# Performance work log

Hardware: AMD Instinct MI355X
Metric: run time of the kernel (lower is better)

The kernel has to match this reference:

```python
import jax, jax.numpy as jnp
import numpy as np

NQUBIT = 24
CHI = 512
Q = 2
MID_SCALE = 1.0 / 32.0  # 1/sqrt(Q*CHI): keeps the sequential bond-matrix product O(1)


def _to_c(x):
    # x[..., 0] = real part, x[..., 1] = imag part -> complex64
    return jax.lax.complex(x[..., 0], x[..., 1])


def setup_inputs() -> dict:
    key = jax.random.key(0)
    k1, k2, k3 = jax.random.split(key, 3)
    t_first = jax.random.normal(k1, (1, Q, CHI, 2), dtype=jnp.float32)
    t_mid = jax.random.normal(k2, (NQUBIT - 2, CHI, Q, CHI, 2), dtype=jnp.float32) * MID_SCALE
    t_last = jax.random.normal(k3, (CHI, Q, 1, 2), dtype=jnp.float32)
    return {"t_first": t_first, "t_mid": t_mid, "t_last": t_last}


def _sweep(t_first, t_mid, t_last):
    # Faithful translation of center_orthogonalization(c=-1):
    # left-to-right orthogonalize_left2right over sites 0..nqubit-2, dc=-1 (no
    # truncation), normalize=False. Each step: SVD of (Dl*q, Dr) reshape,
    # keep u as the new site tensor, absorb r = diag(s) @ vh into the next site
    # via einsum 'ab,bcd->acd'. Returns the center (last) tensor.
    tensors = [_to_c(t_first)] + [_to_c(t_mid[i]) for i in range(NQUBIT - 2)] + [_to_c(t_last)]
    for i in range(NQUBIT - 1):  # loop over sites (structural, shapes differ per site)
        t = tensors[i]
        Dl, q, Dr = t.shape
        u, s, vh = jnp.linalg.svd(t.reshape(Dl * q, Dr), full_matrices=False)
        tensors[i] = u.reshape(Dl, q, -1)            # left-orthogonal site tensor
        r = s.astype(vh.dtype)[:, None] * vh          # diag(s) @ vh, shape (k, Dr)
        tensors[i + 1] = jnp.einsum('ab,bcd->acd', r, tensors[i + 1])
    c = tensors[-1]  # center tensor, shape (CHI, Q, 1) complex64
    return jnp.stack([jnp.real(c), jnp.imag(c)], axis=-1)  # (CHI, Q, 1, 2) float32


def reference(t_first, t_mid, t_last):
    return _sweep(t_first, t_mid, t_last)
```

## Files before the change

### kernel.cpp

```cpp
#include <hip/hip_runtime.h>
#include <math.h>


#define LDV 513
typedef float2 cplx;

__device__ __forceinline__ cplx cmul(cplx a, cplx b){ return make_float2(a.x*b.x - a.y*b.y, a.x*b.y + a.y*b.x); }
__device__ __forceinline__ cplx cmulc(cplx a, cplx b){  return make_float2(a.x*b.x + a.y*b.y, a.x*b.y - a.y*b.x); }
__device__ __forceinline__ cplx cadd(cplx a, cplx b){ return make_float2(a.x+b.x, a.y+b.y); }
__device__ __forceinline__ cplx csub(cplx a, cplx b){ return make_float2(a.x-b.x, a.y-b.y); }
__device__ __forceinline__ cplx conjc(cplx a){ return make_float2(a.x, -a.y); }

#define EPS_S 5.9604645e-8f
#define UNFL_S 1.17549435e-38f
#define UW 256

__device__ cplx g_A[1024*512];
__device__ cplx g_B[512*512];
__device__ cplx g_VTc[512*512];
__device__ cplx g_R[512*512];
__device__ cplx g_tauf[520];
__device__ cplx g_taup[520];
__device__ float g_d[520], g_e[520];
__device__ float g_VTr[LDV*LDV];
__device__ float g_VT2[LDV*LDV];
__device__ float g_W[LDV*LDV];
__device__ float g_z[520], g_zz[520], g_zorig[520], g_dtmp[520], g_ztmp[520], g_dsig[520];
__device__ double g_root[520];
__device__ int g_idxq[520], g_idx[520], g_idxp[520], g_rowmap[520];
__device__ int g_inode[80], g_ndiml[80], g_ndimr[80];
__device__ float g_sig[520];
__device__ int g_K, g_nlvl_, g_nd_;
__device__ float g_tol_, g_z1_;
__device__ double g_rho_;
__device__ float g_scq[520];
__device__ float g_betaq[520];
__device__ float g_rn[520];
__device__ float g_partC[256];
__device__ float g_partR[256];

__device__ __forceinline__ float wred(float v){
  for (int off=32;off;off>>=1) v+=__shfl_down(v,off);
  return v;
}
__device__ __forceinline__ float reduce256(const float* arr){
  __shared__ float sr[256];
  sr[threadIdx.x]=arr[threadIdx.x];
  __syncthreads();
  for (int s=128;s>0;s>>=1){
    if (threadIdx.x<s) sr[threadIdx.x]+=sr[threadIdx.x+s];
    __syncthreads();
  }
  float v=sr[0];
  __syncthreads();
  return v;
}

struct RfgOut { float beta; cplx tau; cplx scal; int skip; };
__device__ RfgOut clarfg_head(cplx alpha, float xn2){
  RfgOut o;
  if (xn2==0.f && alpha.y==0.f){
    o.beta=alpha.x; o.tau=make_float2(0.f,0.f); o.scal=make_float2(0.f,0.f); o.skip=1;
  } else {
    float anorm=sqrtf(alpha.x*alpha.x+alpha.y*alpha.y+xn2);
    float beta=(alpha.x>=0.f)?-anorm:anorm;
    o.beta=beta;
    o.tau=make_float2((beta-alpha.x)/beta,-alpha.y/beta);
    cplx dd=make_float2(alpha.x-beta,alpha.y);
    float dn=dd.x*dd.x+dd.y*dd.y;
    o.scal=make_float2(dd.x/dn,-dd.y/dn);
    o.skip=0;
  }
  return o;
}

__device__ float slapy2(float x, float y){
  float xa=fabsf(x), ya=fabsf(y);
  float w=fmaxf(xa,ya), z=fminf(xa,ya);
  if (z==0.f) return w;
  float q=z/w; return w*sqrtf(1.f+q*q);
}

__device__ void slartg(float f, float g, float* cs, float* sn, float* r){
  if (g==0.f){ *cs=1.f; *sn=0.f; *r=f; }
  else if (f==0.f){ *cs=0.f; *sn=(g>0.f)?1.f:-1.f; *r=fabsf(g); }
  else {
    float f1=fabsf(f);
    float d=sqrtf(f*f+g*g);
    *cs = f1/d;
    *r = (f>0.f)? d : -d;
    *sn = g / *r;
  }
}

__device__ void slas2(float f, float g, float h, float* ssmin, float* ssmax){
  float fa=fabsf(f), ga=fabsf(g), ha=fabsf(h);
  float fhmn=fminf(fa,ha), fhmx=fmaxf(fa,ha);
  if (fhmn==0.f){
    *ssmin=0.f;
    if (fhmx==0.f) *ssmax=ga;
    else { float mx=fmaxf(fhmx,ga), mn=fminf(fhmx,ga); float q=mn/mx; *ssmax=mx*sqrtf(1.f+q*q); }
  } else {
    if (ga < fhmx){
      float as=1.f+fhmn/fhmx, at=(fhmx-fhmn)/fhmx;
      float au=ga/fhmx; au=au*au;
      float c=2.f/(sqrtf(as*as+au)+sqrtf(at*at+au));
      *ssmin=fhmn*c; *ssmax=fhmx/c;
    } else {
      float au=fhmx/ga;
      if (au==0.f){ *ssmin=(fhmn*fhmx)/ga; *ssmax=ga; }
      else {
        float as=1.f+fhmn/fhmx, at=(fhmx-fhmn)/fhmx;
        float c=1.f/(sqrtf(1.f+(as*au)*(as*au))+sqrtf(1.f+(at*au)*(at*au)));
        *ssmin=(fhmn*c)*au; *ssmin=*ssmin+*ssmin;
        *ssmax=ga/(c+c);
      }
    }
  }
}

__device__ void slasv2(float f, float g, float h, float* ssmin, float* ssmax,
                       float* snr, float* csr, float* snl, float* csl){
  float ft=f, fa=fabsf(f), ht=h, ha=fabsf(h);
  int pmax=1;
  bool swap_=(ha>fa);
  if (swap_){ pmax=3; float t=ft; ft=ht; ht=t; t=fa; fa=ha; ha=t; }
  float gt=g, ga=fabsf(g);
  float clt=0.f, crt=0.f, slt=0.f, srt=0.f;
  if (ga==0.f){ *ssmin=ha; *ssmax=fa; clt=1.f; crt=1.f; slt=0.f; srt=0.f; }
  else {
    bool gasmal=true;
    if (ga>fa){
      pmax=2;
      if ((fa/ga) < EPS_S){
        gasmal=false;
        *ssmax=ga;
        if (ha>1.f) *ssmin=fa/(ga/ha); else *ssmin=(fa/ga)*ha;
        clt=1.f; slt=ht/gt; srt=1.f; crt=ft/gt;
      }
    }
    if (gasmal){
      float d=fa-ha;
      float l=(d==fa)?1.f:(d/fa);
      float mm=gt/ft;
      float t=2.f-l;
      float mm2=mm*mm, tt=t*t;
      float s=sqrtf(tt+mm2);
      float r=(l==0.f)?fabsf(mm):sqrtf(l*l+mm2);
      float a=0.5f*(s+r);
      *ssmin=ha/a; *ssmax=fa*a;
      if (mm2==0.f){
        if (l==0.f) t=copysignf(2.f,ft)*copysignf(1.f,gt);
        else t=gt/copysignf(d,ft)+mm/t;
      } else {
        t=(mm/(s+t)+mm/(r+l))*(1.f+a);
      }
      float l2=sqrtf(t*t+4.f);
      crt=2.f/l2; srt=t/l2;
      clt=(crt+srt*mm)/a;
      slt=(ht/ft)*srt/a;
    }
  }
  if (swap_){ *csl=srt; *snl=crt; *csr=slt; *snr=clt; }
  else      { *csl=clt; *snl=slt; *csr=crt; *snr=srt; }
  float tsign=0.f;
  if (pmax==1) tsign=copysignf(1.f,*csr)*copysignf(1.f,*csl)*copysignf(1.f,f);
  if (pmax==2) tsign=copysignf(1.f,*snr)*copysignf(1.f,*csl)*copysignf(1.f,g);
  if (pmax==3) tsign=copysignf(1.f,*snr)*copysignf(1.f,*snl)*copysignf(1.f,h);
  *ssmax=copysignf(*ssmax,tsign);
  *ssmin=copysignf(*ssmin,tsign*copysignf(1.f,f)*copysignf(1.f,h));
}

__device__ void slasr_f(int mrows, int ncols, const float* c1, const float* s1, float* a, int lda){
  for (int j=1;j<=mrows-1;++j){
    float ct=c1[j], st=s1[j];
    if (ct!=1.f || st!=0.f){
      float* rj=&a[(j-1)*lda]; float* rj1=&a[j*lda];
      for (int i=0;i<ncols;++i){
        float tmp=rj1[i];
        rj1[i]=ct*tmp-st*rj[i];
        rj[i]=st*tmp+ct*rj[i];
      }
    }
  }
}
__device__ void slasr_b(int mrows, int ncols, const float* c1, const float* s1, float* a, int lda){
  for (int j=mrows-1;j>=1;--j){
    float ct=c1[j], st=s1[j];
    if (ct!=1.f || st!=0.f){
      float* rj=&a[(j-1)*lda]; float* rj1=&a[j*lda];
      for (int i=0;i<ncols;++i){
        float tmp=rj1[i];
        rj1[i]=ct*tmp-st*rj[i];
        rj[i]=st*tmp+ct*rj[i];
      }
    }
  }
}

__device__ void sbdsqr_u(int n, int ncvt, float* d, float* e, float* vt, int ldvt){
  const int MAXITR=6;
  if (n==0) return;
  if (n>1){
    int nm1=n-1, nm12=nm1+nm1, nm13=nm12+nm1;
    float wk[112];
    float tolmul=10.f;
    float tol=tolmul*EPS_S;
    float smax=0.f;
    for (int i=1;i<=n;i++) smax=fmaxf(smax,fabsf(d[i]));
    for (int i=1;i<=n-1;i++) smax=fmaxf(smax,fabsf(e[i]));
    float sminl=0.f, thresh;
    {
      float sminoa=fabsf(d[1]);
      if (sminoa!=0.f){
        float mu=sminoa;
        for (int i=2;i<=n;i++){
          mu=fabsf(d[i])*(mu/(mu+fabsf(e[i-1])));
          sminoa=fminf(sminoa,mu);
          if (sminoa==0.f) break;
        }
      }
      sminoa=sminoa/sqrtf((float)n);
      thresh=fmaxf(tol*sminoa,(float)(MAXITR*n*n)*UNFL_S);
    }
    int M=n, iter=0, maxit=MAXITR*n*n;
    int oldll=-1, oldm=-1, idir=0;
    while (1){
      if (M<=1) break;
      if (iter>maxit) break;
      int ll=0; bool split=false;
      smax=fabsf(d[M]);
      for (int lll=1;lll<=M-1;++lll){
        ll=M-lll;
        float abss=fabsf(d[ll]), abse=fabsf(e[ll]);
        if (abse<=thresh){ split=true; break; }
        smax=fmaxf(smax,fmaxf(abss,abse));
      }
      if (!split) ll=0;
      else {
        e[ll]=0.f;
        if (ll==M-1){ M=M-1; continue; }
      }
      ll=ll+1;
      if (ll==M-1){
        float sigmn,sigmx,sinr,cosr,sinl,cosl;
        slasv2(d[M-1],e[M-1],d[M],&sigmn,&sigmx,&sinr,&cosr,&sinl,&cosl);
        d[M-1]=sigmx; e[M-1]=0.f; d[M]=sigmn;
        if (ncvt>0){
          float* x=&vt[(M-2)*ldvt]; float* y=&vt[(M-1)*ldvt];
          for (int c=0;c<ncvt;c++){ float xv=x[c],yv=y[c]; x[c]=cosr*xv+sinr*yv; y[c]=cosr*yv-sinr*xv; }
        }
        M-=2; continue;
      }
      if (ll>oldm || M<oldll) idir=(fabsf(d[ll])>=fabsf(d[M]))?1:2;
      bool conv=false;
      if (idir==1){
        if (fabsf(e[M-1])<=fabsf(tol)*fabsf(d[M])){ e[M-1]=0.f; conv=true; }
        else {
          float mu=fabsf(d[ll]); sminl=mu;
          for (int lll=ll;lll<=M-1;++lll){
            if (fabsf(e[lll])<=tol*mu){ e[lll]=0.f; conv=true; break; }
            mu=fabsf(d[lll+1])*(mu/(mu+fabsf(e[lll])));
            sminl=fminf(sminl,mu);
          }
        }
      } else {
        if (fabsf(e[ll])<=fabsf(tol)*fabsf(d[ll])){ e[ll]=0.f; conv=true; }
        else {
          float mu=fabsf(d[M]); sminl=mu;
          for (int lll=M-1;lll>=ll;--lll){
            if (fabsf(e[lll])<=tol*mu){ e[lll]=0.f; conv=true; break; }
            mu=fabsf(d[lll])*(mu/(mu+fabsf(e[lll])));
            sminl=fminf(sminl,mu);
          }
        }
      }
      if (conv) continue;
      oldll=ll; oldm=M;
      float shift=0.f, rr;
      if ((float)n*tol*(sminl/smax)<=fmaxf(EPS_S,0.01f*tol)) shift=0.f;
      else {
        float sll;
        if (idir==1){ sll=fabsf(d[ll]); slas2(d[M-1],e[M-1],d[M],&shift,&rr); }
        else        { sll=fabsf(d[M]);  slas2(d[ll],e[ll],d[ll+1],&shift,&rr); }
        if (sll>0.f){ float q=shift/sll; if (q*q<EPS_S) shift=0.f; }
      }
      iter += M-ll;
      if (shift==0.f){
        if (idir==1){
          float cs=1.f, oldcs=1.f, sn=0.f, oldsn=0.f;
          for (int i=ll;i<=M-1;++i){
            float c2,r1;
            slartg(d[i]*cs,e[i],&c2,&sn,&r1); cs=c2;
            if (i>ll) e[i-1]=oldsn*r1;
            float oc2;
            slartg(oldcs*r1,d[i+1]*sn,&oc2,&oldsn,&d[i]); oldcs=oc2;
            wk[i-ll+1]=cs; wk[i-ll+1+nm1]=sn;
          }
          float h=d[M]*cs; d[M]=h*oldcs; e[M-1]=h*oldsn;
          if (ncvt>0) slasr_f(M-ll+1,ncvt,wk,wk+nm1,&vt[(ll-1)*ldvt],ldvt);
          if (fabsf(e[M-1])<=thresh) e[M-1]=0.f;
        } else {
          float cs=1.f, oldcs=1.f, sn=0.f, oldsn=0.f;
          for (int i=M;i>=ll+1;--i){
            float c2,r1;
            slartg(d[i]*cs,e[i-1],&c2,&sn,&r1); cs=c2;
            if (i<M) e[i]=oldsn*r1;
            float oc2;
            slartg(oldcs*r1,d[i-1]*sn,&oc2,&oldsn,&d[i]); oldcs=oc2;
            wk[i-ll]=cs; wk[i-ll+nm1]=-sn;
            wk[i-ll+nm12]=oldcs; wk[i-ll+nm13]=-oldsn;
          }
          float h=d[ll]*cs; d[ll]=h*oldcs; e[ll]=h*oldsn;
          if (ncvt>0) slasr_b(M-ll+1,ncvt,wk+nm12,wk+nm13,&vt[(ll-1)*ldvt],ldvt);
          if (fabsf(e[ll])<=thresh) e[ll]=0.f;
        }
      } else {
        if (idir==1){
          float f=(fabsf(d[ll])-shift)*(copysignf(1.f,d[ll])+shift/d[ll]);
          float g=e[ll], cosr,sinr,cosl,sinl,r1;
          for (int i=ll;i<=M-1;++i){
            slartg(f,g,&cosr,&sinr,&r1);
            if (i>ll) e[i-1]=r1;
            f=cosr*d[i]+sinr*e[i];
            e[i]=cosr*e[i]-sinr*d[i];
            g=sinr*d[i+1];
            d[i+1]=cosr*d[i+1];
            slartg(f,g,&cosl,&sinl,&r1);
            d[i]=r1;
            f=cosl*e[i]+sinl*d[i+1];
            d[i+1]=cosl*d[i+1]-sinl*e[i];
            if (i<M-1){ g=sinl*e[i+1]; e[i+1]=cosl*e[i+1]; }
            wk[i-ll+1]=cosr; wk[i-ll+1+nm1]=sinr;
            wk[i-ll+1+nm12]=cosl; wk[i-ll+1+nm13]=sinl;
          }
          e[M-1]=f;
          if (ncvt>0) slasr_f(M-ll+1,ncvt,wk,wk+nm1,&vt[(ll-1)*ldvt],ldvt);
          if (fabsf(e[M-1])<=thresh) e[M-1]=0.f;
        } else {
          float f=(fabsf(d[M])-shift)*(copysignf(1.f,d[M])+shift/d[M]);
          float g=e[M-1], cosr,sinr,cosl,sinl,r1;
          for (int i=M;i>=ll+1;--i){
            slartg(f,g,&cosr,&sinr,&r1);
            if (i<M) e[i]=r1;
            f=cosr*d[i]+sinr*e[i-1];
            e[i-1]=cosr*e[i-1]-sinr*d[i];
            g=sinr*d[i-1];
            d[i-1]=cosr*d[i-1];
            slartg(f,g,&cosl,&sinl,&r1);
            d[i]=r1;
            f=cosl*e[i-1]+sinl*d[i-1];
            d[i-1]=cosl*d[i-1]-sinl*e[i-1];
            if (i>ll+1){ g=sinl*e[i-2]; e[i-2]=cosl*e[i-2]; }
            wk[i-ll]=cosr; wk[i-ll+nm1]=-sinr;
            wk[i-ll+nm12]=cosl; wk[i-ll+nm13]=-sinl;
          }
          e[ll]=f;
          if (fabsf(e[ll])<=thresh) e[ll]=0.f;
          if (ncvt>0) slasr_b(M-ll+1,ncvt,wk+nm12,wk+nm13,&vt[(ll-1)*ldvt],ldvt);
        }
      }
    }
  }
  for (int i=1;i<=n;i++){
    if (d[i]<0.f){
      d[i]=-d[i];
      if (ncvt>0){ float* row=&vt[(i-1)*ldvt]; for (int c=0;c<ncvt;c++) row[c]=-row[c]; }
    }
  }
  for (int i=1;i<=n-1;i++){
    int isub=1; float smin2=d[1];
    for (int j=2;j<=n+1-i;j++){ if (d[j]<=smin2){ isub=j; smin2=d[j]; } }
    if (isub!=n+1-i){
      d[isub]=d[n+1-i]; d[n+1-i]=smin2;
      if (ncvt>0){
        float* a=&vt[(isub-1)*ldvt]; float* b=&vt[(n-i)*ldvt];
        for (int c=0;c<ncvt;c++){ float t=a[c]; a[c]=b[c]; b[c]=t; }
      }
    }
  }
}

__device__ void slasdq_u(int sqre, int n, int ncvt, float* d, float* e, float* vt, int ldvt){
  if (n==0) return;
  float cwk[33], swk[33];
  int np1=n+1;
  if (sqre==1){
    for (int i=1;i<=n-1;i++){
      float cs,sn,r; slartg(d[i],e[i],&cs,&sn,&r);
      d[i]=r; e[i]=sn*d[i+1]; d[i+1]=cs*d[i+1];
      cwk[i]=cs; swk[i]=sn;
    }
    { float cs,sn,r; slartg(d[n],e[n],&cs,&sn,&r);
      d[n]=r; e[n]=0.f; cwk[n]=cs; swk[n]=sn; }
    if (ncvt>0) slasr_f(np1,ncvt,cwk,swk,vt,ldvt);
    for (int i=1;i<=n-1;i++){
      float cs,sn,r; slartg(d[i],e[i],&cs,&sn,&r);
      d[i]=r; e[i]=sn*d[i+1]; d[i+1]=cs*d[i+1];
    }
  }
  sbdsqr_u(n,ncvt,d,e,vt,ldvt);
  for (int i=1;i<=n;i++){
    int isub=i; float smin2=d[i];
    for (int j=i+1;j<=n;j++){ if (d[j]<smin2){ isub=j; smin2=d[j]; } }
    if (isub!=i){
      d[isub]=d[i]; d[i]=smin2;
      if (ncvt>0){
        float* a=&vt[(isub-1)*ldvt]; float* b=&vt[(i-1)*ldvt];
        for (int c=0;c<ncvt;c++){ float t=a[c]; a[c]=b[c]; b[c]=t; }
      }
    }
  }
}

__device__ void slamrg(int n1, int n2, const float* a, int s1, int s2, int* idx){
  int n1sv=n1, n2sv=n2, i=1;
  int ind1=(s1>0)?1:n1;
  int ind2=(s2>0)?(1+n1):(n1+n2);
  while (n1sv>0 && n2sv>0){
    if (a[ind1]<=a[ind2]){ idx[i++]=ind1; ind1+=s1; n1sv--; }
    else { idx[i++]=ind2; ind2+=s2; n2sv--; }
  }
  if (n1sv==0){ for(;n2sv>0;n2sv--){ idx[i++]=ind2; ind2+=s2; } }
  else { for(;n1sv>0;n1sv--){ idx[i++]=ind1; ind1+=s1; } }
}

__device__ void slasdt(int n, int* lvl, int* nd, int* inode, int* ndiml, int* ndimr, int msub){
  int maxn=(n>1)?n:1;
  float temp=logf((float)maxn/(float)(msub+1))/logf(2.f);
  *lvl=(int)temp+1;
  int i=n/2;
  inode[1]=i+1; ndiml[1]=i; ndimr[1]=n-i-1;
  int il=0, ir=1, llst=1;
  for (int nl=1;nl<=*lvl-1;++nl){
    for (int j=0;j<=llst-1;++j){
      il+=2; ir+=2;
      int nc=llst+j;
      ndiml[il]=ndiml[nc]/2;
      ndimr[il]=ndiml[nc]-ndiml[il]-1;
      inode[il]=inode[nc]-ndimr[il]-1;
      ndiml[ir]=ndimr[nc]/2;
      ndimr[ir]=ndimr[nc]-ndiml[ir]-1;
      inode[ir]=inode[nc]+ndiml[ir]+1;
    }
    llst*=2;
  }
  *nd=llst*2-1;
}

__device__ void merge_node(int nl, int nr, int sqre, float* d, int* idxq,
                           float alpha, float beta, float* VT, int ld)
{
  const int tid=threadIdx.x, nth=blockDim.x;
  const int n=nl+nr+1, m=n+sqre, nlp1=nl+1, nlp2=nl+2;
  if (tid==0){
    float* z=g_z;
    float z1=alpha*VT[(nlp1-1)*ld+(nlp1-1)];
    z[1]=z1; g_z1_=z1;
    for (int i=nl;i>=1;--i){
      z[i+1]=alpha*VT[(i-1)*ld+(nlp1-1)];
      d[i+1]=d[i];
      idxq[i+1]=idxq[i]+1;
    }
    for (int i=nlp2;i<=m;++i) z[i]=beta*VT[(i-1)*ld+(nlp2-1)];
    d[1]=0.f;
    for (int i=nlp2;i<=n;++i) idxq[i]+=nlp1;
    for (int i=2;i<=n;++i){ g_dtmp[i]=d[idxq[i]]; g_ztmp[i]=z[idxq[i]]; }
    slamrg(nl,nr,g_dtmp+1,1,1,g_idx+1);
    for (int i=2;i<=n;++i){
      int idxi=1+g_idx[i];
      d[i]=g_dtmp[idxi];
      z[i]=g_ztmp[idxi];
    }
    float tol=fmaxf(fabsf(alpha),fabsf(beta));
    tol=8.f*EPS_S*fmaxf(fabsf(d[n]),tol);
    g_tol_=tol;
    int K=1, K2=n+1, jprev=0, j;
    for (j=2;j<=n;++j){
      if (fabsf(z[j])<=tol){
        K2--; g_idxp[K2]=j;
        if (j==n){ jprev=0; break; }
      } else { jprev=j; break; }
    }
    if (jprev>0){
      j=jprev;
      for (;;){
        j++;
        if (j>n) break;
        if (fabsf(z[j])<=tol){ K2--; g_idxp[K2]=j; }
        else {
          if (fabsf(d[j]-d[jprev])<=tol){
            float s_=z[jprev], c_=z[j];
            float tau_=slapy2(c_,s_);
            c_/=tau_; s_=-s_/tau_;
            z[j]=tau_; z[jprev]=0.f;
            int idxjp=idxq[g_idx[jprev]+1];
            int idxj =idxq[g_idx[j]+1];
            if (idxjp<=nlp1) idxjp--;
            if (idxj <=nlp1) idxj--;
            float* xr=&VT[(idxjp-1)*ld];
            float* yr=&VT[(idxj-1)*ld];
            for (int cc=0;cc<m;++cc){
              float xv=xr[cc], yv=yr[cc];
              xr[cc]=c_*xv+s_*yv;
              yr[cc]=c_*yv-s_*xv;
            }
            K2--; g_idxp[K2]=jprev;
            jprev=j;
          } else {
            K++; g_zz[K]=z[jprev]; g_idxp[K]=jprev;
            jprev=j;
          }
        }
      }
      K++; g_zz[K]=z[jprev]; g_idxp[K]=jprev;
    }
    g_K=K;
    for (int jj=2;jj<=n;++jj){
      g_dsig[jj]=d[g_idxp[jj]];
      int rm=idxq[g_idx[g_idxp[jj]]+1];
      if (rm<=nlp1) rm--;
      g_rowmap[jj]=rm;
    }
  }
  __syncthreads();
  int K=g_K;
  for (int t=tid;t<(n-1)*m;t+=nth){
    int jj=2+t/m, cc=t%m;
    g_VT2[(jj-1)*LDV+cc]=VT[(g_rowmap[jj]-1)*ld+cc];
  }
  __syncthreads();
  if (tid==0){
    float tol=g_tol_;
    g_dsig[1]=0.f;
    float hlftol=tol*0.5f;
    if (fabsf(g_dsig[2])<=hlftol) g_dsig[2]=hlftol;
    float z1=g_z1_;
    float c_=1.f, s_=0.f;
    if (m>n){
      float t1=slapy2(z1,g_z[m]);
      if (t1<=tol){ c_=1.f; s_=0.f; g_z[1]=tol; }
      else { g_z[1]=t1; c_=z1/t1; s_=g_z[m]/t1; }
    } else {
      if (fabsf(z1)<=tol) g_z[1]=tol; else g_z[1]=z1;
    }
    for (int jj=2;jj<=K;++jj) g_z[jj]=g_zz[jj];
    if (m>n){
      for (int i=1;i<=nlp1;++i){
        float v=VT[(nlp1-1)*ld+(i-1)];
        VT[(m-1)*ld+(i-1)]=-s_*v;
        g_VT2[(i-1)]=c_*v;
      }
      for (int i=nlp2;i<=m;++i){
        float v=VT[(m-1)*ld+(i-1)];
        g_VT2[(i-1)]=s_*v;
        VT[(m-1)*ld+(i-1)]=c_*v;
      }
    } else {
      for (int i=1;i<=m;++i) g_VT2[(i-1)]=VT[(nlp1-1)*ld+(i-1)];
    }
    for (int jj=K+1;jj<=n;++jj) d[jj]=g_dsig[jj];
    double rho=0.0;
    for (int jj=1;jj<=K;++jj){ double zz2=(double)g_z[jj]; rho+=zz2*zz2; g_zorig[jj]=g_z[jj]; }
    g_rho_=rho;
  }
  __syncthreads();
  for (int t=tid;t<(n-K)*m;t+=nth){
    int jj=K+1+t/m, cc=t%m;
    VT[(jj-1)*ld+cc]=g_VT2[(jj-1)*LDV+cc];
  }
  __syncthreads();
  if (K==1){
    if (tid==0){
      d[1]=fabsf(g_z[1]);
      for (int cc=0;cc<m;++cc) VT[cc]=g_VT2[cc];
      slamrg(1,n-1,d,1,-1,idxq);
    }
    __syncthreads();
    return;
  }
  {
    double rho=g_rho_;
    for (int i=1+tid;i<=K;i+=nth){
      double di=(double)g_dsig[i];
      double lo=di*di, hi;
      if (i<K){ double dn=(double)g_dsig[i+1]; hi=dn*dn; }
      else { double dn=(double)g_dsig[K]; hi=dn*dn+rho; }
      for (int it=0;it<110;++it){
        double mid=0.5*(lo+hi);
        double f=1.0;
        for (int j=1;j<=K;++j){
          double dj=(double)g_dsig[j];
          double zj=(double)g_z[j];
          f+=zj*zj/(dj*dj-mid);
        }
        if (f>=0.0) hi=mid; else lo=mid;
      }
      g_root[i]=0.5*(lo+hi);
      d[i]=(float)sqrt(g_root[i]);
    }
  }
  __syncthreads();
  for (int i=1+tid;i<=K;i+=nth){
    double di=(double)g_dsig[i], di2=di*di;
    double p=di2-g_root[K];
    for (int j=1;j<=i-1;++j){
      double dj=(double)g_dsig[j];
      p*=(di2-g_root[j])/((di-dj)*(di+dj));
    }
    for (int j=i;j<=K-1;++j){
      double dj1=(double)g_dsig[j+1];
      p*=(di2-g_root[j])/((di-dj1)*(di+dj1));
    }
    g_ztmp[i]=copysignf((float)sqrt(fabs(p)),g_zorig[i]);
  }
  __syncthreads();
  for (int i=1+tid;i<=K;i+=nth) g_z[i]=g_ztmp[i];
  __syncthreads();
  for (int i=1+tid;i<=K;i+=nth){
    double xi=g_root[i];
    double nrm=0.0;
    for (int j=1;j<=K;++j){
      double dj=(double)g_dsig[j];
      double w=(double)g_z[j]/(dj*dj-xi);
      g_W[(i-1)*LDV+(j-1)]=(float)w;
      nrm+=w*w;
    }
    float inv=(float)(1.0/sqrt(nrm));
    for (int j=1;j<=K;++j) g_W[(i-1)*LDV+(j-1)]*=inv;
  }
  __syncthreads();
  for (int t=tid;t<K*m;t+=nth){
    int i=1+t/m, cc=t%m;
    float acc=0.f;
    for (int j=1;j<=K;++j)
      acc=fmaf(g_W[(i-1)*LDV+(j-1)],g_VT2[(j-1)*LDV+cc],acc);
    VT[(i-1)*ld+cc]=acc;
  }
  __syncthreads();
  if (tid==0) slamrg(K,n-K,d,1,-1,idxq);
  __syncthreads();
}

__global__ __launch_bounds__(1024) void k_sbdsdc(int n){
  const int tid=threadIdx.x, lane=tid&63, wv=tid>>6;
  for (int t=tid;t<n*n;t+=1024)
    g_VTr[(t/n)*LDV+(t%n)]=((t/n)==(t%n))?1.f:0.f;
  __syncthreads();
  if (n<=25){
    if (tid==0){
      slasdq_u(0,n,n,g_d,g_e,g_VTr,LDV);
      for (int j=1;j<=n;++j) g_idxq[j]=j;
    }
    __syncthreads();
  } else {
    if (tid==0){
      int lvl,nd;
      slasdt(n,&lvl,&nd,g_inode,g_ndiml,g_ndimr,25);
      g_nlvl_=lvl; g_nd_=nd;
    }
    __syncthreads();
    int nd=g_nd_, nlvl=g_nlvl_;
    int ndb1=(nd+1)/2;
    int ntask=(nd-ndb1+1)*2;
    for (int task=wv;task<ntask;task+=16){
      if (lane==0){
        int node=ndb1+(task>>1);
        int ic=g_inode[node], nl=g_ndiml[node], nr=g_ndimr[node];
        if ((task&1)==0){
          int nlf=ic-nl;
          slasdq_u(1,nl,nl+1,g_d+(nlf-1),g_e+(nlf-1),&g_VTr[(nlf-1)*LDV+(nlf-1)],LDV);
          for (int j2=1;j2<=nl;++j2) g_idxq[nlf-1+j2]=j2;
        } else {
          int nrf=ic+1;
          int sq=(node==nd)?0:1;
          slasdq_u(sq,nr,nr+sq,g_d+(nrf-1),g_e+(nrf-1),&g_VTr[(nrf-1)*LDV+(nrf-1)],LDV);
          for (int j2=1;j2<=nr;++j2) g_idxq[nrf-1+j2]=j2;
        }
      }
    }
    __syncthreads();
    for (int lvl=nlvl;lvl>=1;--lvl){
      int lf=(lvl==1)?1:(1<<(lvl-1));
      int llast=(lvl==1)?1:(2*lf-1);
      for (int node=lf;node<=llast;++node){
        int ic=g_inode[node], nl=g_ndiml[node], nr=g_ndimr[node];
        int nlf=ic-nl;
        int sq=(node==llast)?0:1;
        float alpha=g_d[ic], beta=g_e[ic];
        merge_node(nl,nr,sq,g_d+(nlf-1),g_idxq+(nlf-1),alpha,beta,
                   &g_VTr[(nlf-1)*LDV+(nlf-1)],LDV);
      }
    }
  }
  __syncthreads();
  for (int t=tid;t<n*512;t+=1024){
    int i=t/512, c=t%512;
    int o=g_idxq[n-i];
    float v=(c<n)?g_VTr[(o-1)*LDV+c]:0.f;
    g_VTc[i*512+c]=make_float2(v,0.f);
    if (c==0) g_sig[i]=g_d[o];
  }
}

__global__ void k_m0(const float* __restrict__ tf){
  int i=blockIdx.x*blockDim.x+threadIdx.x;
  if (i<1024) g_A[i]=make_float2(tf[2*i],tf[2*i+1]);
}

__global__ __launch_bounds__(1024) void k_lq(int m){
  const int n=512;
  const int tid=threadIdx.x, lane=tid&63, wv=tid>>6;
  __shared__ float s_part[16];
  __shared__ cplx s_tau, s_scal;
  __shared__ float s_beta; __shared__ int s_skip;
  for (int i=1;i<=m;++i){
    for (int c=i+tid;c<=n;c+=1024) g_A[(i-1)*512+(c-1)].y=-g_A[(i-1)*512+(c-1)].y;
    __syncthreads();
    float sq=0.f;
    for (int c=i+1+tid;c<=n;c+=1024){
      cplx a=g_A[(i-1)*512+(c-1)];
      sq=fmaf(a.x,a.x,fmaf(a.y,a.y,sq));
    }
    sq=wred(sq);
    if (lane==0) s_part[wv]=sq;
    __syncthreads();
    if (tid==0){
      float xn2=0.f; for (int w=0;w<16;w++) xn2+=s_part[w];
      RfgOut o=clarfg_head(g_A[(i-1)*512+(i-1)],xn2);
      s_beta=o.beta; s_tau=o.tau; s_scal=o.scal; s_skip=o.skip;
      g_tauf[i]=o.tau;
    }
    __syncthreads();
    if (!s_skip){
      for (int c=i+1+tid;c<=n;c+=1024)
        g_A[(i-1)*512+(c-1)]=cmul(g_A[(i-1)*512+(c-1)],s_scal);
    }
    __syncthreads();
    if (!s_skip){
      cplx tau=s_tau;
      for (int r=i+1+wv;r<=m;r+=16){
        cplx acc=make_float2(0.f,0.f);
        for (int c=i+lane;c<=n;c+=64){
          cplx u=(c==i)?make_float2(1.f,0.f):g_A[(i-1)*512+(c-1)];
          acc=cadd(acc,cmul(g_A[(r-1)*512+(c-1)],u));
        }
        acc.x=wred(acc.x); acc.y=wred(acc.y);
        acc.x=__shfl(acc.x,0); acc.y=__shfl(acc.y,0);
        cplx tw=cmul(tau,acc);
        for (int c=i+lane;c<=n;c+=64){
          cplx u=(c==i)?make_float2(1.f,0.f):g_A[(i-1)*512+(c-1)];
          g_A[(r-1)*512+(c-1)]=csub(g_A[(r-1)*512+(c-1)],cmul(tw,conjc(u)));
        }
      }
    }
    __syncthreads();
    if (tid==0) g_A[(i-1)*512+(i-1)]=make_float2(s_beta,0.f);
    __syncthreads();
  }
}

__global__ void k_copyL(int m){
  int t=blockIdx.x*blockDim.x+threadIdx.x;
  if (t>=m*m) return;
  int r=t/m, c=t%m;
  g_B[r*512+c]=(c<=r)?g_A[r*512+c]:make_float2(0.f,0.f);
}
__global__ void k_copyM(){
  int t=blockIdx.x*blockDim.x+threadIdx.x;
  if (t<512*512) g_B[t]=g_A[t];
}
__global__ void k_copyR_b(){
  int t=blockIdx.x*blockDim.x+threadIdx.x;
  if (t>=512*512) return;
  int r=t/512, c=t%512;
  g_B[t]=(c>r)?g_A[t]:((c==r)?make_float2(g_betaq[r+1],0.f):make_float2(0.f,0.f));
}

__global__ __launch_bounds__(1024) void k_bd(int n){
  const int tid=threadIdx.x, lane=tid&63, wv=tid>>6;
  __shared__ float s_part[16];
  __shared__ cplx s_tau, s_scal;
  __shared__ float s_beta; __shared__ int s_skip;
  for (int i=1;i<=n;++i){
    float sq=0.f;
    for (int r=i+1+tid;r<=n;r+=1024){
      cplx a=g_B[(r-1)*512+(i-1)];
      sq=fmaf(a.x,a.x,fmaf(a.y,a.y,sq));
    }
    sq=wred(sq);
    if (lane==0) s_part[wv]=sq;
    __syncthreads();
    if (tid==0){
      float xn2=0.f; for (int w=0;w<16;w++) xn2+=s_part[w];
      RfgOut o=clarfg_head(g_B[(i-1)*512+(i-1)],xn2);
      s_beta=o.beta; s_tau=o.tau; s_scal=o.scal; s_skip=o.skip;
      g_d[i]=o.beta;
    }
    __syncthreads();
    if (!s_skip){
      for (int r=i+1+tid;r<=n;r+=1024)
        g_B[(r-1)*512+(i-1)]=cmul(g_B[(r-1)*512+(i-1)],s_scal);
    }
    __syncthreads();
    if (!s_skip){
      cplx tauc=conjc(s_tau);
      for (int c=i+1+wv;c<=n;c+=16){
        cplx acc=make_float2(0.f,0.f);
        for (int r=i+lane;r<=n;r+=64){
          cplx v=(r==i)?make_float2(1.f,0.f):g_B[(r-1)*512+(i-1)];
          acc=cadd(acc,cmulc(v,g_B[(r-1)*512+(c-1)]));
        }
        acc.x=wred(acc.x); acc.y=wred(acc.y);
        acc.x=__shfl(acc.x,0); acc.y=__shfl(acc.y,0);
        cplx tw=cmul(tauc,acc);
        for (int r=i+lane;r<=n;r+=64){
          cplx v=(r==i)?make_float2(1.f,0.f):g_B[(r-1)*512+(i-1)];
          g_B[(r-1)*512+(c-1)]=csub(g_B[(r-1)*512+(c-1)],cmul(tw,v));
        }
      }
    }
    __syncthreads();
    if (tid==0) g_B[(i-1)*512+(i-1)]=make_float2(s_beta,0.f);
    __syncthreads();
    if (i<n){
      for (int c=i+1+tid;c<=n;c+=1024) g_B[(i-1)*512+(c-1)].y=-g_B[(i-1)*512+(c-1)].y;
      __syncthreads();
      float sq2=0.f;
      for (int c=i+2+tid;c<=n;c+=1024){
        cplx a=g_B[(i-1)*512+(c-1)];
        sq2=fmaf(a.x,a.x,fmaf(a.y,a.y,sq2));
      }
      sq2=wred(sq2);
      if (lane==0) s_part[wv]=sq2;
      __syncthreads();
      if (tid==0){
        float xn2=0.f; for (int w=0;w<16;w++) xn2+=s_part[w];
        RfgOut o=clarfg_head(g_B[(i-1)*512+(i)],xn2);
        s_beta=o.beta; s_tau=o.tau; s_scal=o.scal; s_skip=o.skip;
        g_e[i]=o.beta; g_taup[i]=o.tau;
      }
      __syncthreads();
      if (!s_skip){
        for (int c=i+2+tid;c<=n;c+=1024)
          g_B[(i-1)*512+(c-1)]=cmul(g_B[(i-1)*512+(c-1)],s_scal);
      }
      __syncthreads();
      if (!s_skip){
        cplx tau=s_tau;
        for (int r=i+1+wv;r<=n;r+=16){
          cplx acc=make_float2(0.f,0.f);
          for (int c=i+1+lane;c<=n;c+=64){
            cplx v=(c==i+1)?make_float2(1.f,0.f):g_B[(i-1)*512+(c-1)];
            acc=cadd(acc,cmul(g_B[(r-1)*512+(c-1)],v));
          }
          acc.x=wred(acc.x); acc.y=wred(acc.y);
          acc.x=__shfl(acc.x,0); acc.y=__shfl(acc.y,0);
          cplx tw=cmul(tau,acc);
          for (int c=i+1+lane;c<=n;c+=64){
            cplx v=(c==i+1)?make_float2(1.f,0.f):g_B[(i-1)*512+(c-1)];
            g_B[(r-1)*512+(c-1)]=csub(g_B[(r-1)*512+(c-1)],cmul(tw,conjc(v)));
          }
        }
      }
      __syncthreads();
      for (int c=i+2+tid;c<=n;c+=1024) g_B[(i-1)*512+(c-1)].y=-g_B[(i-1)*512+(c-1)].y;
      if (tid==0) g_B[(i-1)*512+(i)]=make_float2(s_beta,0.f);
      __syncthreads();
    }
  }
}

__global__ __launch_bounds__(1024) void k_applyPH(int n){
  const int tid=threadIdx.x, lane=tid&63, wv=tid>>6;
  for (int i=n-1;i>=1;--i){
    cplx tau=g_taup[i];
    if (tau.x==0.f && tau.y==0.f) continue;
    cplx tauc=conjc(tau);
    for (int r=1+wv;r<=n;r+=16){
      cplx acc=make_float2(0.f,0.f);
      for (int c=i+1+lane;c<=n;c+=64){
        cplx v=(c==i+1)?make_float2(1.f,0.f):conjc(g_B[(i-1)*512+(c-1)]);
        acc=cadd(acc,cmul(g_VTc[(r-1)*512+(c-1)],v));
      }
      acc.x=wred(acc.x); acc.y=wred(acc.y);
      acc.x=__shfl(acc.x,0); acc.y=__shfl(acc.y,0);
      cplx tw=cmul(tauc,acc);
      for (int c=i+1+lane;c<=n;c+=64){
        cplx vb=(c==i+1)?make_float2(1.f,0.f):g_B[(i-1)*512+(c-1)];
        g_VTc[(r-1)*512+(c-1)]=csub(g_VTc[(r-1)*512+(c-1)],cmul(tw,vb));
      }
    }
    __syncthreads();
  }
}

__global__ __launch_bounds__(1024) void k_applyQlq(int m){
  const int tid=threadIdx.x, lane=tid&63, wv=tid>>6;
  for (int i=m;i>=1;--i){
    cplx tau=g_tauf[i];
    if (tau.x==0.f && tau.y==0.f) continue;
    cplx tauc=conjc(tau);
    for (int r=1+wv;r<=m;r+=16){
      cplx acc=make_float2(0.f,0.f);
      for (int c=i+lane;c<=512;c+=64){
        cplx u=(c==i)?make_float2(1.f,0.f):g_A[(i-1)*512+(c-1)];
        acc=cadd(acc,cmul(g_VTc[(r-1)*512+(c-1)],u));
      }
      acc.x=wred(acc.x); acc.y=wred(acc.y);
      acc.x=__shfl(acc.x,0); acc.y=__shfl(acc.y,0);
      cplx tw=cmul(tauc,acc);
      for (int c=i+lane;c<=512;c+=64){
        cplx u=(c==i)?make_float2(1.f,0.f):g_A[(i-1)*512+(c-1)];
        g_VTc[(r-1)*512+(c-1)]=csub(g_VTc[(r-1)*512+(c-1)],cmul(tw,conjc(u)));
      }
    }
    __syncthreads();
  }
}


__global__ __launch_bounds__(256) void u_qr_pro(){
  __shared__ float sr[256];
  int t=threadIdx.x;
  float sq=0.f;
  for (int r=2+t;r<=1024;r+=256){ cplx a=g_A[(r-1)*512]; sq=fmaf(a.x,a.x,fmaf(a.y,a.y,sq)); }
  sr[t]=sq; __syncthreads();
  for (int s=128;s>0;s>>=1){ if (t<s) sr[t]+=sr[t+s]; __syncthreads(); }
  if (t==0) g_scq[1]=sr[0];
}

__global__ __launch_bounds__(256) void u_qr(int j){
  const int m=1024, n=512;
  int gtid=blockIdx.x*256+threadIdx.x;
  int lane=gtid&63, gw=gtid>>6;
  float xn2=g_scq[j];
  cplx alpha=g_A[(j-1)*512+(j-1)];
  RfgOut o=clarfg_head(alpha,xn2);
  if (gtid==0) g_betaq[j]=o.beta;
  cplx tauc=conjc(o.tau);
  float nsq=0.f;
  for (int c=j+1+gw;c<=n;c+=UW){
    cplx acc=make_float2(0.f,0.f);
    for (int r=j+lane;r<=m;r+=64){
      cplx v=(r==j)?make_float2(1.f,0.f):cmul(g_A[(r-1)*512+(j-1)],o.scal);
      acc=cadd(acc,cmulc(v,g_A[(r-1)*512+(c-1)]));
    }
    acc.x=wred(acc.x); acc.y=wred(acc.y);
    acc.x=__shfl(acc.x,0); acc.y=__shfl(acc.y,0);
    cplx tw=cmul(tauc,acc);
    for (int r=j+lane;r<=m;r+=64){
      cplx v=(r==j)?make_float2(1.f,0.f):cmul(g_A[(r-1)*512+(j-1)],o.scal);
      cplx nv=csub(g_A[(r-1)*512+(c-1)],cmul(tw,v));
      g_A[(r-1)*512+(c-1)]=nv;
      if (c==j+1 && r>=j+2) nsq=fmaf(nv.x,nv.x,fmaf(nv.y,nv.y,nsq));
    }
  }
  if (gw==0){
    nsq=wred(nsq);
    if (lane==0) g_scq[j+1]=nsq;
  }
}

__global__ __launch_bounds__(256) void u_bd_pro(){
  int t=threadIdx.x;
  float sq=0.f;
  for (int r=2+t;r<=512;r+=256){ cplx a=g_B[(r-1)*512]; sq=fmaf(a.x,a.x,fmaf(a.y,a.y,sq)); }
  g_partR[t]=sq;
}

__global__ __launch_bounds__(256) void u_bd_col(int i){
  const int n=512;
  float xn2c=reduce256(g_partR);
  int gtid=blockIdx.x*256+threadIdx.x;
  int lane=gtid&63, gw=gtid>>6;
  cplx alpha=g_B[(i-1)*512+(i-1)];
  RfgOut oc=clarfg_head(alpha,xn2c);
  if (gtid==0) g_d[i]=oc.beta;
  cplx tauc=conjc(oc.tau);
  float nsqA=0.f;
  for (int c=i+1+gw;c<=n;c+=UW){
    cplx acc=make_float2(0.f,0.f);
    for (int r=i+lane;r<=n;r+=64){
      cplx v=(r==i)?make_float2(1.f,0.f):cmul(g_B[(r-1)*512+(i-1)],oc.scal);
      acc=cadd(acc,cmulc(v,g_B[(r-1)*512+(c-1)]));
    }
    acc.x=wred(acc.x); acc.y=wred(acc.y);
    acc.x=__shfl(acc.x,0); acc.y=__shfl(acc.y,0);
    cplx tw=cmul(tauc,acc);
    for (int r=i+lane;r<=n;r+=64){
      cplx v=(r==i)?make_float2(1.f,0.f):cmul(g_B[(r-1)*512+(i-1)],oc.scal);
      cplx nv=csub(g_B[(r-1)*512+(c-1)],cmul(tw,v));
      g_B[(r-1)*512+(c-1)]=nv;
      if (r==i && c>=i+2) nsqA=fmaf(nv.x,nv.x,fmaf(nv.y,nv.y,nsqA));
    }
  }
  if (lane==0) g_partC[gw]=nsqA;
}

__global__ __launch_bounds__(256) void u_bd_row(int i){
  const int n=512;
  float xn2r=reduce256(g_partC);
  int gtid=blockIdx.x*256+threadIdx.x;
  int lane=gtid&63, gw=gtid>>6;
  cplx alphar=conjc(g_B[(i-1)*512+(i)]);
  RfgOut orr=clarfg_head(alphar,xn2r);
  if (gtid==0){ g_e[i]=orr.beta; g_taup[i]=orr.tau; g_rn[i]=xn2r; }
  float nsqB=0.f;
  for (int r=i+1+gw;r<=n;r+=UW){
    cplx acc=make_float2(0.f,0.f);
    for (int c=i+1+lane;c<=n;c+=64){
      cplx v=(c==i+1)?make_float2(1.f,0.f):cmul(conjc(g_B[(i-1)*512+(c-1)]),orr.scal);
      acc=cadd(acc,cmul(g_B[(r-1)*512+(c-1)],v));
    }
    acc.x=wred(acc.x); acc.y=wred(acc.y);
    acc.x=__shfl(acc.x,0); acc.y=__shfl(acc.y,0);
    cplx tw=cmul(orr.tau,acc);
    for (int c=i+1+lane;c<=n;c+=64){
      cplx v=(c==i+1)?make_float2(1.f,0.f):cmul(conjc(g_B[(i-1)*512+(c-1)]),orr.scal);
      cplx nv=csub(g_B[(r-1)*512+(c-1)],cmul(tw,conjc(v)));
      g_B[(r-1)*512+(c-1)]=nv;
      if (c==i+1 && r>=i+2) nsqB=fmaf(nv.x,nv.x,fmaf(nv.y,nv.y,nsqB));
    }
  }
  if (lane==0) g_partR[gw]=nsqB;
}

__global__ __launch_bounds__(256) void u_ph(){
  const int n=512;
  int b=blockIdx.x;
  int wv=threadIdx.x>>6, lane=threadIdx.x&63;
  int r0=b*8+wv*2;
  for (int i=n-1;i>=1;--i){
    cplx alphar=conjc(g_B[(i-1)*512+(i)]);
    RfgOut o=clarfg_head(alphar,g_rn[i]);
    if (o.skip) continue;
    cplx tauc=conjc(o.tau);
    for (int rr=0;rr<2;++rr){
      int r=r0+rr+1;
      cplx acc=make_float2(0.f,0.f);
      for (int c=i+1+lane;c<=n;c+=64){
        cplx v=(c==i+1)?make_float2(1.f,0.f):cmul(conjc(g_B[(i-1)*512+(c-1)]),o.scal);
        acc=cadd(acc,cmul(g_VTc[(r-1)*512+(c-1)],v));
      }
      acc.x=wred(acc.x); acc.y=wred(acc.y);
      acc.x=__shfl(acc.x,0); acc.y=__shfl(acc.y,0);
      cplx tw=cmul(tauc,acc);
      for (int c=i+1+lane;c<=n;c+=64){
        cplx v=(c==i+1)?make_float2(1.f,0.f):cmul(conjc(g_B[(i-1)*512+(c-1)]),o.scal);
        g_VTc[(r-1)*512+(c-1)]=csub(g_VTc[(r-1)*512+(c-1)],cmul(tw,conjc(v)));
      }
    }
  }
}

__global__ void k_formR(int kk){
  int t=blockIdx.x*blockDim.x+threadIdx.x;
  if (t>=kk*512) return;
  float s=g_sig[t/512];
  cplx v=g_VTc[t];
  g_R[t]=make_float2(s*v.x,s*v.y);
}

__global__ void k_next(const float* __restrict__ tmid, int site){
  int row=blockIdx.x;
  int a=row>>1, s=row&1;
  int b=blockIdx.y*blockDim.x+threadIdx.x;
  const float* base=tmid+(size_t)site*512*2*512*2;
  cplx acc=make_float2(0.f,0.f);
  for (int c=0;c<512;++c){
    cplx r=g_R[a*512+c];
    size_t off=((((size_t)c)*2+s)*512+b)*2;
    cplx x=make_float2(base[off],base[off+1]);
    acc=cadd(acc,cmul(r,x));
  }
  g_A[row*512+b]=acc;
}

__global__ void k_final(const float* __restrict__ tlast, float* __restrict__ out){
  int a=blockIdx.x*blockDim.x+threadIdx.x;
  if (a>=512) return;
  for (int s=0;s<2;++s){
    cplx acc=make_float2(0.f,0.f);
    for (int c=0;c<512;++c){
      cplx r=g_R[a*512+c];
      cplx x=make_float2(tlast[(c*2+s)*2],tlast[(c*2+s)*2+1]);
      acc=cadd(acc,cmul(r,x));
    }
    out[a*4+s*2+0]=acc.x;
    out[a*4+s*2+1]=acc.y;
  }
}

extern "C" void kernel_launch(void* const* d_in, const int* in_sizes, int n_in,
                              void* d_out, int out_size, void* d_ws, size_t ws_size,
                              hipStream_t stream) {
  const float* t_first=(const float*)d_in[0];
  const float* t_mid  =(const float*)d_in[1];
  const float* t_last =(const float*)d_in[2];
  float* out=(float*)d_out;
  (void)in_sizes; (void)n_in; (void)d_ws; (void)ws_size; (void)out_size;

  k_m0<<<dim3(4),256,0,stream>>>(t_first);

  int rows=2;
  for (int site=0;site<23;++site){
    int mm=rows;
    int nb=(mm<512)?mm:512;
    if (mm<512){
      k_lq<<<1,1024,0,stream>>>(mm);
      k_copyL<<<dim3((mm*mm+255)/256),256,0,stream>>>(mm);
      k_bd<<<1,1024,0,stream>>>(mm);
      k_sbdsdc<<<1,1024,0,stream>>>(mm);
      k_applyPH<<<1,1024,0,stream>>>(mm);
      k_applyQlq<<<1,1024,0,stream>>>(mm);
    } else {
      if (mm==512){
        k_copyM<<<dim3((512*512+255)/256),256,0,stream>>>();
      } else {
        u_qr_pro<<<1,256,0,stream>>>();
        for (int j=1;j<=512;++j) u_qr<<<64,256,0,stream>>>(j);
        k_copyR_b<<<dim3((512*512+255)/256),256,0,stream>>>();
      }
      u_bd_pro<<<1,256,0,stream>>>();
      for (int i=1;i<=512;++i){
        u_bd_col<<<64,256,0,stream>>>(i);
        if (i<512) u_bd_row<<<64,256,0,stream>>>(i);
      }
      k_sbdsdc<<<1,1024,0,stream>>>(512);
      u_ph<<<64,256,0,stream>>>();
    }
    k_formR<<<dim3((nb*512+255)/256),256,0,stream>>>(nb);
    if (site<22){
      k_next<<<dim3(2*nb,2),256,0,stream>>>(t_mid,site);
      rows=2*nb;
    } else {
      k_final<<<dim3(2),256,0,stream>>>(t_last,out);
    }
  }
}
```

Before: 1.194 s.

## Panel the Householder QR and finish small bidiagonalization in one block

The QR loop, which launched one kernel per column, now processes 64-column panels. A single-block kernel factors each panel and a multi-block kernel applies the panel's reflectors to the trailing columns, so the launch count drops from 512 to about 16. The bidiagonalization keeps per-column multi-block launches only for the first 128 steps. The remaining steps run inside one 1024-thread block with __syncthreads, avoiding hundreds of small launches where the trailing matrix is small. The trade-offs are single-block execution for the tail, and each column being re-read once per reflector in the apply kernel.

```diff
diff --git a/kernel.cpp b/kernel.cpp
--- a/kernel.cpp
+++ b/kernel.cpp
@@ -14,6 +14,7 @@
 #define EPS_S 5.9604645e-8f
 #define UNFL_S 1.17549435e-38f
 #define UW 256
+#define IBD 129
 
 __device__ cplx g_A[1024*512];
 __device__ cplx g_B[512*512];
@@ -930,37 +931,78 @@
   if (t==0) g_scq[1]=sr[0];
 }
 
-__global__ __launch_bounds__(256) void u_qr(int j){
+__global__ __launch_bounds__(1024) void p_qr_panel(int j0){
+  const int m=1024;
+  const int tid=threadIdx.x, lane=tid&63, wv=tid>>6;
+  __shared__ float s_x;
+  if (tid==0) s_x=g_scq[j0];
+  __syncthreads();
+  for (int jl=0;jl<64;++jl){
+    int j=j0+jl;
+    float xn2=s_x;
+    cplx alpha=g_A[(j-1)*512+(j-1)];
+    RfgOut o=clarfg_head(alpha,xn2);
+    if (tid==0) g_betaq[j]=o.beta;
+    __syncthreads();
+    cplx tauc=conjc(o.tau);
+    int cend=j0+63;
+    for (int c=j+1+wv;c<=cend;c+=16){
+      cplx acc=make_float2(0.f,0.f);
+      for (int r=j+lane;r<=m;r+=64){
+        cplx v=(r==j)?make_float2(1.f,0.f):cmul(g_A[(r-1)*512+(j-1)],o.scal);
+        acc=cadd(acc,cmulc(v,g_A[(r-1)*512+(c-1)]));
+      }
+      acc.x=wred(acc.x); acc.y=wred(acc.y);
+      acc.x=__shfl(acc.x,0); acc.y=__shfl(acc.y,0);
+      cplx tw=cmul(tauc,acc);
+      float nsq=0.f;
+      for (int r=j+lane;r<=m;r+=64){
+        cplx v=(r==j)?make_float2(1.f,0.f):cmul(g_A[(r-1)*512+(j-1)],o.scal);
+        cplx nv=csub(g_A[(r-1)*512+(c-1)],cmul(tw,v));
+        g_A[(r-1)*512+(c-1)]=nv;
+        if (c==j+1 && r>=j+2) nsq=fmaf(nv.x,nv.x,fmaf(nv.y,nv.y,nsq));
+      }
+      if (c==j+1){
+        nsq=wred(nsq);
+        if (lane==0){ s_x=nsq; g_scq[j+1]=nsq; }
+      }
+    }
+    __syncthreads();
+  }
+}
+
+__global__ __launch_bounds__(256) void p_qr_apply(int j0){
   const int m=1024, n=512;
-  int gtid=blockIdx.x*256+threadIdx.x;
-  int lane=gtid&63, gw=gtid>>6;
-  float xn2=g_scq[j];
-  cplx alpha=g_A[(j-1)*512+(j-1)];
-  RfgOut o=clarfg_head(alpha,xn2);
-  if (gtid==0) g_betaq[j]=o.beta;
-  cplx tauc=conjc(o.tau);
-  float nsq=0.f;
-  for (int c=j+1+gw;c<=n;c+=UW){
-    cplx acc=make_float2(0.f,0.f);
-    for (int r=j+lane;r<=m;r+=64){
-      cplx v=(r==j)?make_float2(1.f,0.f):cmul(g_A[(r-1)*512+(j-1)],o.scal);
-      acc=cadd(acc,cmulc(v,g_A[(r-1)*512+(c-1)]));
-    }
-    acc.x=wred(acc.x); acc.y=wred(acc.y);
-    acc.x=__shfl(acc.x,0); acc.y=__shfl(acc.y,0);
-    cplx tw=cmul(tauc,acc);
-    for (int r=j+lane;r<=m;r+=64){
-      cplx v=(r==j)?make_float2(1.f,0.f):cmul(g_A[(r-1)*512+(j-1)],o.scal);
-      cplx nv=csub(g_A[(r-1)*512+(c-1)],cmul(tw,v));
-      g_A[(r-1)*512+(c-1)]=nv;
-      if (c==j+1 && r>=j+2) nsq=fmaf(nv.x,nv.x,fmaf(nv.y,nv.y,nsq));
-    }
-  }
-  if (gw==0){
-    nsq=wred(nsq);
-    if (lane==0) g_scq[j+1]=nsq;
-  }
-}
+  const int gtid=blockIdx.x*256+threadIdx.x;
+  const int lane=gtid&63, gw=gtid>>6;
+  for (int c=j0+64+gw;c<=n;c+=UW){
+    for (int jl=0;jl<64;++jl){
+      int j=j0+jl;
+      RfgOut o=clarfg_head(g_A[(j-1)*512+(j-1)], g_scq[j]);
+      cplx tauc=conjc(o.tau);
+      cplx acc=make_float2(0.f,0.f);
+      for (int r=j+lane;r<=m;r+=64){
+        cplx v=(r==j)?make_float2(1.f,0.f):cmul(g_A[(r-1)*512+(j-1)],o.scal);
+        acc=cadd(acc,cmulc(v,g_A[(r-1)*512+(c-1)]));
+      }
+      acc.x=wred(acc.x); acc.y=wred(acc.y);
+      acc.x=__shfl(acc.x,0); acc.y=__shfl(acc.y,0);
+      cplx tw=cmul(tauc,acc);
+      float nsq=0.f;
+      for (int r=j+lane;r<=m;r+=64){
+        cplx v=(r==j)?make_float2(1.f,0.f):cmul(g_A[(r-1)*512+(j-1)],o.scal);
+        cplx nv=csub(g_A[(r-1)*512+(c-1)],cmul(tw,v));
+        g_A[(r-1)*512+(c-1)]=nv;
+        if (c==j+1 && r>=j+2) nsq=fmaf(nv.x,nv.x,fmaf(nv.y,nv.y,nsq));
+      }
+      if (c==j+1 && jl==63){
+        nsq=wred(nsq);
+        if (lane==0) g_scq[j+1]=nsq;
+      }
+    }
+  }
+}
+
 
 __global__ __launch_bounds__(256) void u_bd_pro(){
   int t=threadIdx.x;
@@ -1024,6 +1066,71 @@
     }
   }
   if (lane==0) g_partR[gw]=nsqB;
+}
+
+__global__ __launch_bounds__(1024) void u_bd_tail(int i0){
+  const int n=512;
+  const int tid=threadIdx.x, lane=tid&63, wv=tid>>6;
+  __shared__ float s_p[16];
+  __shared__ float sr[256];
+  if (tid<256) sr[tid]=g_partR[tid];
+  __syncthreads();
+  for (int s=128;s>0;s>>=1){ if (tid<s) sr[tid]+=sr[tid+s]; __syncthreads(); }
+  float xn2c=sr[0];
+  for (int i=i0;i<=n;++i){
+    cplx alpha=g_B[(i-1)*512+(i-1)];
+    RfgOut oc=clarfg_head(alpha,xn2c);
+    if (tid==0) g_d[i]=oc.beta;
+    __syncthreads();
+    cplx tauc=conjc(oc.tau);
+    float nsqA=0.f;
+    for (int c=i+1+wv;c<=n;c+=16){
+      cplx acc=make_float2(0.f,0.f);
+      for (int r=i+lane;r<=n;r+=64){
+        cplx v=(r==i)?make_float2(1.f,0.f):cmul(g_B[(r-1)*512+(i-1)],oc.scal);
+        acc=cadd(acc,cmulc(v,g_B[(r-1)*512+(c-1)]));
+      }
+      acc.x=wred(acc.x); acc.y=wred(acc.y);
+      acc.x=__shfl(acc.x,0); acc.y=__shfl(acc.y,0);
+      cplx tw=cmul(tauc,acc);
+      for (int r=i+lane;r<=n;r+=64){
+        cplx v=(r==i)?make_float2(1.f,0.f):cmul(g_B[(r-1)*512+(i-1)],oc.scal);
+        cplx nv=csub(g_B[(r-1)*512+(c-1)],cmul(tw,v));
+        g_B[(r-1)*512+(c-1)]=nv;
+        if (r==i && c>=i+2) nsqA=fmaf(nv.x,nv.x,fmaf(nv.y,nv.y,nsqA));
+      }
+    }
+    if (lane==0) s_p[wv]=nsqA;
+    __syncthreads();
+    if (i==n) break;
+    float xn2r=0.f;
+    for (int w=0;w<16;++w) xn2r+=s_p[w];
+    cplx alphar=conjc(g_B[(i-1)*512+(i)]);
+    RfgOut orr=clarfg_head(alphar,xn2r);
+    if (tid==0){ g_e[i]=orr.beta; g_taup[i]=orr.tau; g_rn[i]=xn2r; }
+    __syncthreads();
+    float nsqB=0.f;
+    for (int r=i+1+wv;r<=n;r+=16){
+      cplx acc=make_float2(0.f,0.f);
+      for (int c=i+1+lane;c<=n;c+=64){
+        cplx v=(c==i+1)?make_float2(1.f,0.f):cmul(conjc(g_B[(i-1)*512+(c-1)]),orr.scal);
+        acc=cadd(acc,cmul(g_B[(r-1)*512+(c-1)],v));
+      }
+      acc.x=wred(acc.x); acc.y=wred(acc.y);
+      acc.x=__shfl(acc.x,0); acc.y=__shfl(acc.y,0);
+      cplx tw=cmul(orr.tau,acc);
+      for (int c=i+1+lane;c<=n;c+=64){
+        cplx v=(c==i+1)?make_float2(1.f,0.f):cmul(conjc(g_B[(i-1)*512+(c-1)]),orr.scal);
+        cplx nv=csub(g_B[(r-1)*512+(c-1)],cmul(tw,conjc(v)));
+        g_B[(r-1)*512+(c-1)]=nv;
+        if (c==i+1 && r>=i+2) nsqB=fmaf(nv.x,nv.x,fmaf(nv.y,nv.y,nsqB));
+      }
+    }
+    if (lane==0) s_p[wv]=nsqB;
+    __syncthreads();
+    xn2c=0.f;
+    for (int w=0;w<16;++w) xn2c+=s_p[w];
+  }
 }
 
 __global__ __launch_bounds__(256) void u_ph(){
@@ -1119,14 +1226,19 @@
         k_copyM<<<dim3((512*512+255)/256),256,0,stream>>>();
       } else {
         u_qr_pro<<<1,256,0,stream>>>();
-        for (int j=1;j<=512;++j) u_qr<<<64,256,0,stream>>>(j);
+        for (int p=0;p<8;++p){
+          int j0=1+64*p;
+          p_qr_panel<<<1,1024,0,stream>>>(j0);
+          if (p<7) p_qr_apply<<<64,256,0,stream>>>(j0);
+        }
         k_copyR_b<<<dim3((512*512+255)/256),256,0,stream>>>();
       }
       u_bd_pro<<<1,256,0,stream>>>();
-      for (int i=1;i<=512;++i){
+      for (int i=1;i<IBD;++i){
         u_bd_col<<<64,256,0,stream>>>(i);
-        if (i<512) u_bd_row<<<64,256,0,stream>>>(i);
-      }
+        u_bd_row<<<64,256,0,stream>>>(i);
+      }
+      u_bd_tail<<<1,1024,0,stream>>>(IBD);
       k_sbdsdc<<<1,1024,0,stream>>>(512);
       u_ph<<<64,256,0,stream>>>();
     }
```

After: 2.516 s. 111% more time.
